# Performance work log

Measured on AMD Instinct MI355X. Metric: run time of the kernel, lower is better.

The kernel has to match this reference:

```python
import jax, jax.numpy as jnp
import numpy as np

N_LEVELS = 16
N_FEAT = 2
LOG2_T = 19
T = 2 ** LOG2_T
BASE_RES = 2 ** 4
MAX_RES = 2 ** 11
PER_LEVEL_SCALE = np.exp((np.log(MAX_RES) - np.log(BASE_RES)) / (N_LEVELS - 1))
RESOLUTIONS = [int(np.floor(BASE_RES * PER_LEVEL_SCALE ** lv)) + 1 for lv in range(N_LEVELS)]
INIT_ACTIVE_LEVEL = 8
N_POINTS = 1048576
N_OUT = N_LEVELS * N_FEAT
# tcnn spatial hashing primes
P1 = jnp.uint32(2654435761)
P2 = jnp.uint32(805459861)


def _level_lookup(x, tbl, res):
    """x: [N,3] in [0,1], tbl: [T,F], res: python int grid resolution."""
    pos = x * (res - 1)                       # [N,3]
    c0 = jnp.clip(jnp.floor(pos).astype(jnp.int32), 0, res - 2)
    w = pos - c0.astype(pos.dtype)            # [N,3] trilinear fractions
    feats = jnp.zeros((x.shape[0], tbl.shape[-1]), dtype=tbl.dtype)
    dense = (res ** 3) <= T                   # static per level: dense grid vs hashed
    for dz in (0, 1):
        for dy in (0, 1):
            for dx in (0, 1):
                offs = jnp.array([dx, dy, dz], jnp.int32)
                c = c0 + offs                 # [N,3] corner int coords
                if dense:
                    idx = c[:, 0] + res * (c[:, 1] + res * c[:, 2])
                else:
                    cu = c.astype(jnp.uint32)
                    idx = ((cu[:, 0]) ^ (cu[:, 1] * P1) ^ (cu[:, 2] * P2)) & jnp.uint32(T - 1)
                    idx = idx.astype(jnp.int32)
                # trilinear corner weight: prod over axes of (w if offs==1 else 1-w)
                wc = jnp.prod(jnp.where(offs == 1, w, 1.0 - w), axis=-1)  # [N]
                feats = feats + tbl[idx] * wc[:, None]
    return feats


def setup_inputs() -> dict:
    key = jax.random.key(0)
    k1, k2 = jax.random.split(key)
    x = jax.random.uniform(k1, (N_POINTS, 3), dtype=jnp.float32)
    # tcnn-style small uniform init of the hash table
    table = jax.random.uniform(k2, (N_LEVELS, T, N_FEAT), dtype=jnp.float32,
                               minval=-1e-4, maxval=1e-4)
    mask = jnp.concatenate([
        jnp.ones(INIT_ACTIVE_LEVEL * N_FEAT, jnp.float32),
        jnp.zeros((N_LEVELS - INIT_ACTIVE_LEVEL) * N_FEAT, jnp.float32),
    ])
    return {"x": x, "table": table, "mask": mask}


def reference(x, table, mask):
    # multi-resolution hash grid encoding + progressive level mask
    outs = [_level_lookup(x, table[lv], RESOLUTIONS[lv]) for lv in range(N_LEVELS)]
    enc = jnp.concatenate(outs, axis=-1)      # [N, 32]
    return enc * mask
```

## Files before the change

### kernel.cpp

```cpp
#include <hip/hip_runtime.h>
#include <cstdint>
#include <cstddef>


namespace {

constexpr int      kNLevels = 16;
constexpr uint32_t kT       = 1u << 19;
constexpr uint32_t kP1      = 2654435761u;
constexpr uint32_t kP2      = 805459861u;

__device__ constexpr int kRes[kNLevels] = {
    17, 23, 31, 43, 59, 81, 112, 154, 213, 295, 407, 562, 777, 1073, 1483, 2049
};

__global__ __launch_bounds__(256) void hashgrid_encode_kernel(
    const float* __restrict__ x,
    const float* __restrict__ table,
    const float* __restrict__ mask,
    float* __restrict__ out,
    int n)
{
    const int p = blockIdx.x * blockDim.x + threadIdx.x;
    if (p >= n) return;

    const float px = x[3 * p + 0];
    const float py = x[3 * p + 1];
    const float pz = x[3 * p + 2];

    float4 o[8];

#pragma unroll
    for (int lv = 0; lv < kNLevels; ++lv) {
        const float m0 = mask[2 * lv + 0];
        const float m1 = mask[2 * lv + 1];
        float r0 = 0.0f, r1 = 0.0f;

        if (m0 != 0.0f || m1 != 0.0f) {
            const int  res   = kRes[lv];
            const bool dense = ((long long)res * res * res) <= (long long)kT;
            const float s = (float)(res - 1);

            const float fx = px * s;
            const float fy = py * s;
            const float fz = pz * s;

            int cx = (int)floorf(fx);
            int cy = (int)floorf(fy);
            int cz = (int)floorf(fz);
            cx = min(max(cx, 0), res - 2);
            cy = min(max(cy, 0), res - 2);
            cz = min(max(cz, 0), res - 2);

            const float wx = fx - (float)cx;
            const float wy = fy - (float)cy;
            const float wz = fz - (float)cz;
            const float ux = 1.0f - wx;
            const float uy = 1.0f - wy;
            const float uz = 1.0f - wz;

            const float* __restrict__ tbl = table + (size_t)lv * (size_t)(kT * 2);

            float2 v[8];
            float  w8[8];
#pragma unroll
            for (int c = 0; c < 8; ++c) {
                const int dx = c & 1;
                const int dy = (c >> 1) & 1;
                const int dz = (c >> 2) & 1;
                const int ix = cx + dx;
                const int iy = cy + dy;
                const int iz = cz + dz;
                uint32_t idx;
                if (dense) {
                    idx = (uint32_t)(ix + res * (iy + res * iz));
                } else {
                    idx = (((uint32_t)ix) ^ ((uint32_t)iy * kP1) ^ ((uint32_t)iz * kP2))
                          & (kT - 1u);
                }
                v[c]  = *(const float2*)(tbl + 2u * idx);
                w8[c] = (dx ? wx : ux) * (dy ? wy : uy) * (dz ? wz : uz);
            }
#pragma unroll
            for (int c = 0; c < 8; ++c) {
                r0 = fmaf(v[c].x, w8[c], r0);
                r1 = fmaf(v[c].y, w8[c], r1);
            }
            r0 *= m0;
            r1 *= m1;
        }

        if (lv & 1) {
            o[lv >> 1].z = r0;
            o[lv >> 1].w = r1;
        } else {
            o[lv >> 1].x = r0;
            o[lv >> 1].y = r1;
        }
    }

    float4* __restrict__ op = (float4*)(out + (size_t)p * 32);
#pragma unroll
    for (int i = 0; i < 8; ++i) op[i] = o[i];
}

}

extern "C" void kernel_launch(void* const* d_in, const int* in_sizes, int n_in,
                              void* d_out, int out_size, void* d_ws, size_t ws_size,
                              hipStream_t stream) {
    const float* x     = (const float*)d_in[0];
    const float* table = (const float*)d_in[1];
    const float* mask  = (const float*)d_in[2];
    float*       out   = (float*)d_out;

    const int n = in_sizes[0] / 3;
    const int block = 256;
    const int grid  = (n + block - 1) / block;
    hashgrid_encode_kernel<<<grid, block, 0, stream>>>(x, table, mask, out, n);
}
```

Measured before the change: 391.0 us.

## Split encoding into dense, per-level hashed, and gather kernels via workspace

Replaces the single fused kernel with three launches. One kernel handles the five dense levels per point, a second runs one grid slice per hashed level so each slice's gathers stay within a single level's table for better cache locality, and a third masks the per-level results from the workspace and writes them interleaved. The aim is to raise L2 hit rates on the random table gathers. The cost is an extra round trip of the full intermediate through workspace memory plus more launches and repeated x loads. Nontemporal loads and stores are also added, and the original fused kernel remains as a fallback when the workspace is too small.

```diff
diff --git a/kernel.cpp b/kernel.cpp
--- a/kernel.cpp
+++ b/kernel.cpp
@@ -10,96 +10,160 @@
 constexpr uint32_t kP1      = 2654435761u;
 constexpr uint32_t kP2      = 805459861u;
 
+typedef float v2f __attribute__((ext_vector_type(2)));
+typedef float v4f __attribute__((ext_vector_type(4)));
+
 __device__ constexpr int kRes[kNLevels] = {
     17, 23, 31, 43, 59, 81, 112, 154, 213, 295, 407, 562, 777, 1073, 1483, 2049
 };
 
-__global__ __launch_bounds__(256) void hashgrid_encode_kernel(
-    const float* __restrict__ x,
-    const float* __restrict__ table,
-    const float* __restrict__ mask,
-    float* __restrict__ out,
-    int n)
+__device__ inline void corner_setup(float px, float py, float pz, int res,
+                                    int& cx, int& cy, int& cz,
+                                    float& wx, float& wy, float& wz) {
+    const float s = (float)(res - 1);
+    const float fx = px * s, fy = py * s, fz = pz * s;
+    cx = (int)floorf(fx); cy = (int)floorf(fy); cz = (int)floorf(fz);
+    cx = min(max(cx, 0), res - 2);
+    cy = min(max(cy, 0), res - 2);
+    cz = min(max(cz, 0), res - 2);
+    wx = fx - (float)cx; wy = fy - (float)cy; wz = fz - (float)cz;
+}
+
+__global__ __launch_bounds__(256) void dense_levels_kernel(
+    const float* __restrict__ x, const float* __restrict__ table,
+    const float* __restrict__ mask, float* __restrict__ ws, int n)
+{
+    const int p = blockIdx.x * blockDim.x + threadIdx.x;
+    if (p >= n) return;
+    const float px = __builtin_nontemporal_load(x + 3 * p + 0);
+    const float py = __builtin_nontemporal_load(x + 3 * p + 1);
+    const float pz = __builtin_nontemporal_load(x + 3 * p + 2);
+
+#pragma unroll
+    for (int lv = 0; lv < 5; ++lv) {
+        const float m0 = mask[2 * lv], m1 = mask[2 * lv + 1];
+        if (m0 == 0.0f && m1 == 0.0f) continue;
+        const int res = kRes[lv];
+        int cx, cy, cz; float wx, wy, wz;
+        corner_setup(px, py, pz, res, cx, cy, cz, wx, wy, wz);
+        const float ux = 1.0f - wx, uy = 1.0f - wy, uz = 1.0f - wz;
+        const float* __restrict__ tbl = table + (size_t)lv * (size_t)(kT * 2);
+        float r0 = 0.0f, r1 = 0.0f;
+#pragma unroll
+        for (int c = 0; c < 8; ++c) {
+            const int dx = c & 1, dy = (c >> 1) & 1, dz = (c >> 2) & 1;
+            const uint32_t idx =
+                (uint32_t)((cx + dx) + res * ((cy + dy) + res * (cz + dz)));
+            const v2f v = *(const v2f*)(tbl + 2u * idx);
+            const float w = (dx ? wx : ux) * (dy ? wy : uy) * (dz ? wz : uz);
+            r0 = fmaf(v.x, w, r0);
+            r1 = fmaf(v.y, w, r1);
+        }
+        v2f o; o.x = r0; o.y = r1;
+        __builtin_nontemporal_store(o, (v2f*)(ws + ((size_t)lv * n + p) * 2));
+    }
+}
+
+__global__ __launch_bounds__(256) void hashed_level_kernel(
+    const float* __restrict__ x, const float* __restrict__ table,
+    const float* __restrict__ mask, float* __restrict__ ws, int n)
+{
+    const int lv = 5 + blockIdx.y;
+    const float m0 = mask[2 * lv], m1 = mask[2 * lv + 1];
+    if (m0 == 0.0f && m1 == 0.0f) return;
+
+    const int p = blockIdx.x * blockDim.x + threadIdx.x;
+    if (p >= n) return;
+    const float px = __builtin_nontemporal_load(x + 3 * p + 0);
+    const float py = __builtin_nontemporal_load(x + 3 * p + 1);
+    const float pz = __builtin_nontemporal_load(x + 3 * p + 2);
+
+    const int res = kRes[lv];
+    int cx, cy, cz; float wx, wy, wz;
+    corner_setup(px, py, pz, res, cx, cy, cz, wx, wy, wz);
+    const float ux = 1.0f - wx, uy = 1.0f - wy, uz = 1.0f - wz;
+    const float* __restrict__ tbl = table + (size_t)lv * (size_t)(kT * 2);
+
+    float r0 = 0.0f, r1 = 0.0f;
+#pragma unroll
+    for (int c = 0; c < 8; ++c) {
+        const int dx = c & 1, dy = (c >> 1) & 1, dz = (c >> 2) & 1;
+        const uint32_t idx =
+            (((uint32_t)(cx + dx)) ^ ((uint32_t)(cy + dy) * kP1)
+                                   ^ ((uint32_t)(cz + dz) * kP2)) & (kT - 1u);
+        const v2f v = *(const v2f*)(tbl + 2u * idx);
+        const float w = (dx ? wx : ux) * (dy ? wy : uy) * (dz ? wz : uz);
+        r0 = fmaf(v.x, w, r0);
+        r1 = fmaf(v.y, w, r1);
+    }
+    v2f o; o.x = r0; o.y = r1;
+    __builtin_nontemporal_store(o, (v2f*)(ws + ((size_t)lv * n + p) * 2));
+}
+
+__global__ __launch_bounds__(256) void gather_out_kernel(
+    const float* __restrict__ ws, const float* __restrict__ mask,
+    float* __restrict__ out, int n)
 {
     const int p = blockIdx.x * blockDim.x + threadIdx.x;
     if (p >= n) return;
 
-    const float px = x[3 * p + 0];
-    const float py = x[3 * p + 1];
-    const float pz = x[3 * p + 2];
-
-    float4 o[8];
-
+    v4f o[8];
 #pragma unroll
     for (int lv = 0; lv < kNLevels; ++lv) {
-        const float m0 = mask[2 * lv + 0];
-        const float m1 = mask[2 * lv + 1];
+        const float m0 = mask[2 * lv], m1 = mask[2 * lv + 1];
         float r0 = 0.0f, r1 = 0.0f;
+        if (m0 != 0.0f || m1 != 0.0f) {
+            const v2f v = __builtin_nontemporal_load(
+                (const v2f*)(ws + ((size_t)lv * n + p) * 2));
+            r0 = v.x * m0;
+            r1 = v.y * m1;
+        }
+        if (lv & 1) { o[lv >> 1].z = r0; o[lv >> 1].w = r1; }
+        else        { o[lv >> 1].x = r0; o[lv >> 1].y = r1; }
+    }
+    v4f* __restrict__ op = (v4f*)(out + (size_t)p * 32);
+#pragma unroll
+    for (int i = 0; i < 8; ++i) __builtin_nontemporal_store(o[i], op + i);
+}
 
+__global__ __launch_bounds__(256) void fused_kernel(
+    const float* __restrict__ x, const float* __restrict__ table,
+    const float* __restrict__ mask, float* __restrict__ out, int n)
+{
+    const int p = blockIdx.x * blockDim.x + threadIdx.x;
+    if (p >= n) return;
+    const float px = x[3 * p + 0], py = x[3 * p + 1], pz = x[3 * p + 2];
+    v4f o[8];
+#pragma unroll
+    for (int lv = 0; lv < kNLevels; ++lv) {
+        const float m0 = mask[2 * lv], m1 = mask[2 * lv + 1];
+        float r0 = 0.0f, r1 = 0.0f;
         if (m0 != 0.0f || m1 != 0.0f) {
-            const int  res   = kRes[lv];
+            const int res = kRes[lv];
             const bool dense = ((long long)res * res * res) <= (long long)kT;
-            const float s = (float)(res - 1);
-
-            const float fx = px * s;
-            const float fy = py * s;
-            const float fz = pz * s;
-
-            int cx = (int)floorf(fx);
-            int cy = (int)floorf(fy);
-            int cz = (int)floorf(fz);
-            cx = min(max(cx, 0), res - 2);
-            cy = min(max(cy, 0), res - 2);
-            cz = min(max(cz, 0), res - 2);
-
-            const float wx = fx - (float)cx;
-            const float wy = fy - (float)cy;
-            const float wz = fz - (float)cz;
-            const float ux = 1.0f - wx;
-            const float uy = 1.0f - wy;
-            const float uz = 1.0f - wz;
-
+            int cx, cy, cz; float wx, wy, wz;
+            corner_setup(px, py, pz, res, cx, cy, cz, wx, wy, wz);
+            const float ux = 1.0f - wx, uy = 1.0f - wy, uz = 1.0f - wz;
             const float* __restrict__ tbl = table + (size_t)lv * (size_t)(kT * 2);
-
-            float2 v[8];
-            float  w8[8];
 #pragma unroll
             for (int c = 0; c < 8; ++c) {
-                const int dx = c & 1;
-                const int dy = (c >> 1) & 1;
-                const int dz = (c >> 2) & 1;
-                const int ix = cx + dx;
-                const int iy = cy + dy;
-                const int iz = cz + dz;
+                const int dx = c & 1, dy = (c >> 1) & 1, dz = (c >> 2) & 1;
+                const int ix = cx + dx, iy = cy + dy, iz = cz + dz;
                 uint32_t idx;
-                if (dense) {
-                    idx = (uint32_t)(ix + res * (iy + res * iz));
-                } else {
-                    idx = (((uint32_t)ix) ^ ((uint32_t)iy * kP1) ^ ((uint32_t)iz * kP2))
-                          & (kT - 1u);
-                }
-                v[c]  = *(const float2*)(tbl + 2u * idx);
-                w8[c] = (dx ? wx : ux) * (dy ? wy : uy) * (dz ? wz : uz);
+                if (dense) idx = (uint32_t)(ix + res * (iy + res * iz));
+                else idx = (((uint32_t)ix) ^ ((uint32_t)iy * kP1)
+                                           ^ ((uint32_t)iz * kP2)) & (kT - 1u);
+                const v2f v = *(const v2f*)(tbl + 2u * idx);
+                const float w = (dx ? wx : ux) * (dy ? wy : uy) * (dz ? wz : uz);
+                r0 = fmaf(v.x, w, r0);
+                r1 = fmaf(v.y, w, r1);
             }
-#pragma unroll
-            for (int c = 0; c < 8; ++c) {
-                r0 = fmaf(v[c].x, w8[c], r0);
-                r1 = fmaf(v[c].y, w8[c], r1);
-            }
-            r0 *= m0;
-            r1 *= m1;
+            r0 *= m0; r1 *= m1;
         }
-
-        if (lv & 1) {
-            o[lv >> 1].z = r0;
-            o[lv >> 1].w = r1;
-        } else {
-            o[lv >> 1].x = r0;
-            o[lv >> 1].y = r1;
-        }
+        if (lv & 1) { o[lv >> 1].z = r0; o[lv >> 1].w = r1; }
+        else        { o[lv >> 1].x = r0; o[lv >> 1].y = r1; }
     }
-
-    float4* __restrict__ op = (float4*)(out + (size_t)p * 32);
+    v4f* __restrict__ op = (v4f*)(out + (size_t)p * 32);
 #pragma unroll
     for (int i = 0; i < 8; ++i) op[i] = o[i];
 }
@@ -116,6 +180,16 @@
 
     const int n = in_sizes[0] / 3;
     const int block = 256;
-    const int grid  = (n + block - 1) / block;
-    hashgrid_encode_kernel<<<grid, block, 0, stream>>>(x, table, mask, out, n);
+    const int gx = (n + block - 1) / block;
+
+    const size_t ws_needed = (size_t)kNLevels * (size_t)n * 2 * sizeof(float);
+    if (ws_size >= ws_needed) {
+        float* ws = (float*)d_ws;
+        dense_levels_kernel<<<gx, block, 0, stream>>>(x, table, mask, ws, n);
+        dim3 grid_h(gx, kNLevels - 5);
+        hashed_level_kernel<<<grid_h, block, 0, stream>>>(x, table, mask, ws, n);
+        gather_out_kernel<<<gx, block, 0, stream>>>(ws, mask, out, n);
+    } else {
+        fused_kernel<<<gx, block, 0, stream>>>(x, table, mask, out, n);
+    }
 }
```

New measurement: 557.2 us. 42.5% more time.
